# Optimization experiments

Measured on AMD Instinct MI355X. Metric: run time of the kernel, lower is better.

The kernel has to match this reference:

```python
import jax, jax.numpy as jnp
import numpy as np

S, H, W = 64, 294, 518
FOCAL = 300.0


def setup_inputs() -> dict:
    key = jax.random.key(0)
    k1, k2, k3, k4, k5, k6 = jax.random.split(key, 6)
    images = jax.random.uniform(k1, (S, 3, H, W), jnp.float32)
    # sample 3D points inside each camera frustum so most project in-frame
    z = jax.random.uniform(k2, (S, H, W), jnp.float32, 1.0, 5.0)
    x = jax.random.uniform(k3, (S, H, W), jnp.float32, -0.9, 0.9) * z * (W / (2.0 * FOCAL))
    y = jax.random.uniform(k4, (S, H, W), jnp.float32, -0.9, 0.9) * z * (H / (2.0 * FOCAL))
    world_points = jnp.stack([x, y, z], axis=-1)
    world_points_conf = jax.random.uniform(k5, (S, H, W), jnp.float32)
    E = jnp.concatenate([jnp.eye(3, dtype=jnp.float32), jnp.zeros((3, 1), jnp.float32)], axis=1)
    extrinsic = jnp.tile(E[None], (S, 1, 1)) + 0.01 * jax.random.normal(k6, (S, 3, 4), jnp.float32)
    K = jnp.array([[FOCAL, 0.0, W / 2.0], [0.0, FOCAL, H / 2.0], [0.0, 0.0, 1.0]], jnp.float32)
    intrinsic = jnp.tile(K[None], (S, 1, 1))
    return dict(images=images, world_points=world_points,
                world_points_conf=world_points_conf,
                extrinsic=extrinsic, intrinsic=intrinsic)


def reference(images, world_points, world_points_conf, extrinsic, intrinsic):
    s, c, h, w = images.shape
    n = s * h * w
    dtype = images.dtype
    # world -> camera -> pixel (per-frame matmul == torch's gather+bmm since
    # every point's b_idx is its own frame)
    pts_h = jnp.concatenate([world_points, jnp.ones((s, h, w, 1), dtype)], axis=-1)
    cam = jnp.einsum('sij,shwj->shwi', extrinsic, pts_h)          # (S,H,W,3)
    z = cam[..., 2].reshape(n)
    uvh = jnp.einsum('sij,shwj->shwi', intrinsic, cam).reshape(n, 3)
    uv = uvh[:, :2] / (uvh[:, 2:] + 1e-7)
    u, v = uv[:, 0], uv[:, 1]
    valid = (z > 0) & (u >= 0) & (u < w) & (v >= 0) & (v < h)
    u = jnp.clip(u, 0, w - 1)
    v = jnp.clip(v, 0, h - 1)
    u0 = u.astype(jnp.int32)
    v0 = v.astype(jnp.int32)
    u1 = jnp.minimum(u0 + 1, w - 1)
    v1 = jnp.minimum(v0 + 1, h - 1)
    du = u - u0.astype(dtype)
    dv = v - v0.astype(dtype)
    vm = valid.astype(dtype)
    w00 = (1 - du) * (1 - dv) * vm
    w01 = (1 - du) * dv * vm
    w10 = du * (1 - dv) * vm
    w11 = du * dv * vm
    base = jnp.repeat(jnp.arange(s, dtype=jnp.int32), h * w) * (h * w)
    pix_idx = base + v0 * w + u0
    # atomic z-buffer: scatter-min of depth, then hit test
    depth_buf = jnp.full((n,), jnp.inf, jnp.float32).at[pix_idx].min(z)
    hit = ((z == depth_buf[pix_idx]) & valid).astype(dtype)
    rgb = images.transpose(0, 2, 3, 1).reshape(n, 3)
    conf = world_points_conf.reshape(n)
    rgb_buf = jnp.zeros((n, 3), dtype)
    conf_buf = jnp.zeros((n,), dtype)
    for wgt, pu, pv in ((w00, u0, v0), (w01, u0, v1), (w10, u1, v0), (w11, u1, v1)):
        pix = base + pv * w + pu
        wh = wgt * hit
        rgb_buf = rgb_buf.at[pix].add(wh[:, None] * rgb)
        conf_buf = conf_buf.at[pix].add(wh * conf)
    over_exposed = (rgb_buf > 1.0).any(axis=1)
    rgb_buf = jnp.clip(rgb_buf, 0.0, 1.0)
    rgb_map = rgb_buf.reshape(s, h, w, 3).transpose(0, 3, 1, 2)
    depth_map = depth_buf.reshape(s, h, w, 1).transpose(0, 3, 1, 2)
    conf_map = conf_buf.reshape(s, h, w, 1).transpose(0, 3, 1, 2)
    mask_map = ((depth_buf < jnp.inf) & ~over_exposed).reshape(s, 1, h, w).astype(jnp.float32)
    return rgb_map, depth_map, conf_map, mask_map
```

## Files before the change

kernel.cpp:

```cpp
#include <hip/hip_runtime.h>
#include <stdint.h>

constexpr int S = 64, H = 294, W = 518;
constexpr int HW = H * W;
constexpr int N = S * HW;

constexpr int BLK = 256;
constexpr int BPF = (HW + BLK - 1) / BLK;
constexpr int NB  = BPF * S;
constexpr int NXCD = 8;

#define DEPTH_MISS 1.0e30f

typedef unsigned long long u64;
constexpr u64 KEY_SENT = 0xFFFFFFFFFFFFFFFFull;

__device__ __forceinline__ int swz_block() {
  const int orig = blockIdx.x;
  return (orig % NXCD) * (NB / NXCD) + orig / NXCD;
}

__device__ __forceinline__ uint32_t enc_f32(float f) {
  uint32_t u = __float_as_uint(f);
  return (u & 0x80000000u) ? ~u : (u | 0x80000000u);
}
__device__ __forceinline__ float dec_f32(uint32_t u) {
  uint32_t b = (u & 0x80000000u) ? (u ^ 0x80000000u) : ~u;
  return __uint_as_float(b);
}

struct Proj {
  float z, du, dv;
  int u0, v0, u1, v1;
  bool valid;
};

__device__ __forceinline__ Proj project(float px, float py, float pz,
                                        const float* __restrict__ E,
                                        const float* __restrict__ K) {
  Proj r;
  float cx = __fmaf_rn(E[0], px, __fmaf_rn(E[1], py, __fmaf_rn(E[2], pz, E[3])));
  float cy = __fmaf_rn(E[4], px, __fmaf_rn(E[5], py, __fmaf_rn(E[6], pz, E[7])));
  float cz = __fmaf_rn(E[8], px, __fmaf_rn(E[9], py, __fmaf_rn(E[10], pz, E[11])));
  float uh = __fmaf_rn(K[0], cx, __fmaf_rn(K[1], cy, __fmul_rn(K[2], cz)));
  float vh = __fmaf_rn(K[3], cx, __fmaf_rn(K[4], cy, __fmul_rn(K[5], cz)));
  float wh = __fmaf_rn(K[6], cx, __fmaf_rn(K[7], cy, __fmul_rn(K[8], cz)));
  float d  = __fadd_rn(wh, 1e-7f);
  float u  = __fdiv_rn(uh, d);
  float v  = __fdiv_rn(vh, d);
  r.z = cz;
  r.valid = (cz > 0.0f) & (u >= 0.0f) & (u < (float)W) & (v >= 0.0f) & (v < (float)H);
  u = fminf(fmaxf(u, 0.0f), (float)(W - 1));
  v = fminf(fmaxf(v, 0.0f), (float)(H - 1));
  int u0 = (int)u;
  int v0 = (int)v;
  r.u0 = u0; r.v0 = v0;
  r.u1 = min(u0 + 1, W - 1);
  r.v1 = min(v0 + 1, H - 1);
  r.du = __fadd_rn(u, -(float)u0);
  r.dv = __fadd_rn(v, -(float)v0);
  return r;
}


__global__ __launch_bounds__(256) void k_prep(
    const float* __restrict__ wp, const float* __restrict__ extr,
    const float* __restrict__ intr, const float* __restrict__ images,
    const float* __restrict__ conf, u64* __restrict__ keys,
    float4* __restrict__ pack4, float2* __restrict__ pack2) {
  const int wg = swz_block();
  const int s  = wg / BPF;
  const int p  = (wg - s * BPF) * BLK + threadIdx.x;
  if (p >= HW) return;
  const float* E = extr + s * 12;
  const float* K = intr + s * 9;
  const int idx = s * HW + p;
  Proj pr = project(wp[idx*3], wp[idx*3+1], wp[idx*3+2], E, K);
  const int pix = s * HW + pr.v0 * W + pr.u0;
  const u64 key = ((u64)enc_f32(pr.z) << 32) | (uint32_t)p;
  atomicMin(&keys[pix], key);

  const size_t ib = (size_t)s * 3 * HW + p;
  const float vf = pr.valid ? 1.f : 0.f;
  float4 c;
  c.x = vf * images[ib];
  c.y = vf * images[ib + HW];
  c.z = vf * images[ib + 2 * HW];
  c.w = vf * conf[idx];
  pack4[idx] = c;
  pack2[idx] = make_float2(vf * pr.du, vf * pr.dv);
}

__global__ __launch_bounds__(256) void k_gather2(
    const u64* __restrict__ keys, const float4* __restrict__ pack4,
    const float2* __restrict__ pack2, float* __restrict__ out) {
  const int wg = swz_block();
  const int s  = wg / BPF;
  const int p  = (wg - s * BPF) * BLK + threadIdx.x;
  if (p >= HW) return;
  const int y = p / W;
  const int x = p - y * W;
  const bool ex = (x == W - 1);
  const bool ey = (y == H - 1);
  const u64* kfr = keys + (size_t)s * HW;

  const u64 kC = kfr[p];
  const u64 kL = kfr[x > 0 ? p - 1 : p];
  const u64 kU = kfr[y > 0 ? p - W : p];
  const u64 kD = kfr[(x > 0 && y > 0) ? p - W - 1 : p];

  const float fC = (kC != KEY_SENT) ? 1.f : 0.f;
  const float fL = (x > 0 && kL != KEY_SENT) ? 1.f : 0.f;
  const float fU = (y > 0 && kU != KEY_SENT) ? 1.f : 0.f;
  const float fD = (x > 0 && y > 0 && kD != KEY_SENT) ? 1.f : 0.f;

  const int base = s * HW;
  const int pC = base + (kC == KEY_SENT ? 0 : (int)(uint32_t)kC);
  const int pL = base + (kL == KEY_SENT ? 0 : (int)(uint32_t)kL);
  const int pU = base + (kU == KEY_SENT ? 0 : (int)(uint32_t)kU);
  const int pD = base + (kD == KEY_SENT ? 0 : (int)(uint32_t)kD);

  const float4 cC = pack4[pC], cL = pack4[pL], cU = pack4[pU], cD = pack4[pD];
  const float2 dC = pack2[pC], dL = pack2[pL], dU = pack2[pU], dD = pack2[pD];

  const float wC = fC * (ex ? 1.f : 1.f - dC.x) * (ey ? 1.f : 1.f - dC.y);
  const float wL = fL * dL.x * (ey ? 1.f : 1.f - dL.y);
  const float wU = fU * (ex ? 1.f : 1.f - dU.x) * dU.y;
  const float wD = fD * dD.x * dD.y;

  const float ar = wC * cC.x + wU * cU.x + wL * cL.x + wD * cD.x;
  const float ag = wC * cC.y + wU * cU.y + wL * cL.y + wD * cD.y;
  const float ab = wC * cC.z + wU * cU.z + wL * cL.z + wD * cD.z;
  const float ac = wC * cC.w + wU * cU.w + wL * cL.w + wD * cD.w;

  const bool over = (ar > 1.f) | (ag > 1.f) | (ab > 1.f);

  float* rgb   = out;
  float* depth = out + (size_t)3 * N;
  float* cbuf  = out + (size_t)4 * N;
  float* mask  = out + (size_t)5 * N;

  const size_t ob = (size_t)s * 3 * HW + p;
  rgb[ob]          = fminf(fmaxf(ar, 0.f), 1.f);
  rgb[ob + HW]     = fminf(fmaxf(ag, 0.f), 1.f);
  rgb[ob + 2 * HW] = fminf(fmaxf(ab, 0.f), 1.f);

  const int i = s * HW + p;
  const bool missed = (kC == KEY_SENT);
  depth[i] = missed ? DEPTH_MISS : dec_f32((uint32_t)(kC >> 32));
  cbuf[i]  = ac;
  mask[i]  = (!missed && !over) ? 1.f : 0.f;
}


__global__ __launch_bounds__(256) void k_depth64(
    const float* __restrict__ wp, const float* __restrict__ extr,
    const float* __restrict__ intr, u64* __restrict__ keys) {
  const int wg = swz_block();
  const int s  = wg / BPF;
  const int p  = (wg - s * BPF) * BLK + threadIdx.x;
  if (p >= HW) return;
  const float* E = extr + s * 12;
  const float* K = intr + s * 9;
  const int idx = s * HW + p;
  Proj pr = project(wp[idx*3], wp[idx*3+1], wp[idx*3+2], E, K);
  const int pix = s * HW + pr.v0 * W + pr.u0;
  const u64 key = ((u64)enc_f32(pr.z) << 32) | (uint32_t)p;
  atomicMin(&keys[pix], key);
}

__global__ __launch_bounds__(256) void k_gather(
    const float* __restrict__ wp, const float* __restrict__ extr,
    const float* __restrict__ intr, const float* __restrict__ images,
    const float* __restrict__ conf, const u64* __restrict__ keys,
    float* __restrict__ out) {
  const int wg = swz_block();
  const int s  = wg / BPF;
  const int p  = (wg - s * BPF) * BLK + threadIdx.x;
  if (p >= HW) return;
  const int y = p / W;
  const int x = p - y * W;
  const float* E = extr + s * 12;
  const float* K = intr + s * 9;
  const u64* kfr = keys + (size_t)s * HW;
  const float* img = images + (size_t)s * 3 * HW;
  const float* cfp = conf + (size_t)s * HW;
  const bool ex = (x == W - 1);
  const bool ey = (y == H - 1);

  float ar = 0.f, ag = 0.f, ab = 0.f, ac = 0.f;
  const u64 k0 = kfr[p];

  auto contrib = [&](u64 k, int role) {
    if (k == KEY_SENT) return;
    const int pid = (int)(uint32_t)k;
    const float* q = wp + ((size_t)s * HW + pid) * 3;
    Proj pr = project(q[0], q[1], q[2], E, K);
    if (!pr.valid) return;
    const float du = pr.du, dv = pr.dv;
    float wgt;
    if (role == 0)      wgt = (ex ? 1.f : 1.f - du) * (ey ? 1.f : 1.f - dv);
    else if (role == 1) wgt = du * (ey ? 1.f : 1.f - dv);
    else if (role == 2) wgt = (ex ? 1.f : 1.f - du) * dv;
    else                wgt = du * dv;
    if (wgt == 0.f) return;
    ar += wgt * img[pid];
    ag += wgt * img[HW + pid];
    ab += wgt * img[2 * HW + pid];
    ac += wgt * cfp[pid];
  };

  contrib(k0, 0);
  if (x > 0)          contrib(kfr[p - 1], 1);
  if (y > 0)          contrib(kfr[p - W], 2);
  if (x > 0 && y > 0) contrib(kfr[p - W - 1], 3);

  const bool over = (ar > 1.f) | (ag > 1.f) | (ab > 1.f);

  float* rgb   = out;
  float* depth = out + (size_t)3 * N;
  float* cbuf  = out + (size_t)4 * N;
  float* mask  = out + (size_t)5 * N;

  const size_t ob = (size_t)s * 3 * HW + p;
  rgb[ob]          = fminf(fmaxf(ar, 0.f), 1.f);
  rgb[ob + HW]     = fminf(fmaxf(ag, 0.f), 1.f);
  rgb[ob + 2 * HW] = fminf(fmaxf(ab, 0.f), 1.f);

  const int i = s * HW + p;
  const bool missed = (k0 == KEY_SENT);
  depth[i] = missed ? DEPTH_MISS : dec_f32((uint32_t)(k0 >> 32));
  cbuf[i]  = ac;
  mask[i]  = (!missed && !over) ? 1.f : 0.f;
}


__global__ __launch_bounds__(256) void k_depth(
    const float* __restrict__ wp, const float* __restrict__ extr,
    const float* __restrict__ intr, uint32_t* __restrict__ denc) {
  const int s = blockIdx.y;
  const int p = blockIdx.x * blockDim.x + threadIdx.x;
  if (p >= HW) return;
  const float* E = extr + s * 12;
  const float* K = intr + s * 9;
  const int idx = s * HW + p;
  Proj pr = project(wp[idx*3], wp[idx*3+1], wp[idx*3+2], E, K);
  const int pix = s * HW + pr.v0 * W + pr.u0;
  atomicMin(&denc[pix], enc_f32(pr.z));
}

__global__ __launch_bounds__(256) void k_splat(
    const float* __restrict__ wp, const float* __restrict__ extr,
    const float* __restrict__ intr, const float* __restrict__ images,
    const float* __restrict__ conf, const uint32_t* __restrict__ denc,
    float* __restrict__ rgb_buf, float* __restrict__ conf_buf) {
  const int s = blockIdx.y;
  const int p = blockIdx.x * blockDim.x + threadIdx.x;
  if (p >= HW) return;
  const float* E = extr + s * 12;
  const float* K = intr + s * 9;
  const int idx = s * HW + p;
  Proj pr = project(wp[idx*3], wp[idx*3+1], wp[idx*3+2], E, K);
  const int pix0 = s * HW + pr.v0 * W + pr.u0;
  if (!pr.valid) return;
  if (enc_f32(pr.z) != denc[pix0]) return;

  const float du = pr.du, dv = pr.dv;
  const float w00 = (1.0f - du) * (1.0f - dv);
  const float w01 = (1.0f - du) * dv;
  const float w10 = du * (1.0f - dv);
  const float w11 = du * dv;

  const int ibase = s * 3 * HW + p;
  const float r = images[ibase];
  const float g = images[ibase + HW];
  const float b = images[ibase + 2 * HW];
  const float cf = conf[idx];
  const int sbase = s * HW;
  const int cbase = s * 3 * HW;

  #define SPLAT(WGT, PU, PV)                                              \
    if ((WGT) != 0.0f) {                                                  \
      const int q = (PV) * W + (PU);                                      \
      unsafeAtomicAdd(&rgb_buf[cbase + q],          (WGT) * r);           \
      unsafeAtomicAdd(&rgb_buf[cbase + HW + q],     (WGT) * g);           \
      unsafeAtomicAdd(&rgb_buf[cbase + 2 * HW + q], (WGT) * b);           \
      unsafeAtomicAdd(&conf_buf[sbase + q],         (WGT) * cf);          \
    }
  SPLAT(w00, pr.u0, pr.v0)
  SPLAT(w01, pr.u0, pr.v1)
  SPLAT(w10, pr.u1, pr.v0)
  SPLAT(w11, pr.u1, pr.v1)
  #undef SPLAT
}

__global__ __launch_bounds__(256) void k_final(float* __restrict__ out) {
  const int s = blockIdx.y;
  const int p = blockIdx.x * blockDim.x + threadIdx.x;
  if (p >= HW) return;
  float* rgb = out;
  float* depth = out + (size_t)3 * N;
  float* mask = out + (size_t)5 * N;
  uint32_t* denc = (uint32_t*)depth;

  const int cbase = s * 3 * HW + p;
  const float r = rgb[cbase];
  const float g = rgb[cbase + HW];
  const float b = rgb[cbase + 2 * HW];
  const bool over = (r > 1.0f) | (g > 1.0f) | (b > 1.0f);
  rgb[cbase]          = fminf(fmaxf(r, 0.0f), 1.0f);
  rgb[cbase + HW]     = fminf(fmaxf(g, 0.0f), 1.0f);
  rgb[cbase + 2 * HW] = fminf(fmaxf(b, 0.0f), 1.0f);

  const int i = s * HW + p;
  const uint32_t u = denc[i];
  const bool missed = (u == 0xFFFFFFFFu);
  depth[i] = missed ? DEPTH_MISS : dec_f32(u);
  mask[i] = (!missed && !over) ? 1.0f : 0.0f;
}

extern "C" void kernel_launch(void* const* d_in, const int* in_sizes, int n_in,
                              void* d_out, int out_size, void* d_ws, size_t ws_size,
                              hipStream_t stream) {
  const float* images = (const float*)d_in[0];
  const float* wp     = (const float*)d_in[1];
  const float* conf   = (const float*)d_in[2];
  const float* extr   = (const float*)d_in[3];
  const float* intr   = (const float*)d_in[4];
  float* out = (float*)d_out;

  const size_t keys_bytes  = (size_t)N * sizeof(u64);
  const size_t pack4_bytes = (size_t)N * sizeof(float4);
  const size_t pack2_bytes = (size_t)N * sizeof(float2);
  dim3 blk(BLK, 1, 1);

  if (ws_size >= keys_bytes + pack4_bytes + pack2_bytes) {
    u64*    keys  = (u64*)d_ws;
    float4* pack4 = (float4*)((char*)d_ws + keys_bytes);
    float2* pack2 = (float2*)((char*)d_ws + keys_bytes + pack4_bytes);
    hipMemsetAsync(keys, 0xFF, keys_bytes, stream);
    dim3 grd(NB, 1, 1);
    hipLaunchKernelGGL(k_prep, grd, blk, 0, stream, wp, extr, intr, images,
                       conf, keys, pack4, pack2);
    hipLaunchKernelGGL(k_gather2, grd, blk, 0, stream, keys, pack4, pack2, out);
  } else if (ws_size >= keys_bytes) {
    u64* keys = (u64*)d_ws;
    hipMemsetAsync(keys, 0xFF, keys_bytes, stream);
    dim3 grd(NB, 1, 1);
    hipLaunchKernelGGL(k_depth64, grd, blk, 0, stream, wp, extr, intr, keys);
    hipLaunchKernelGGL(k_gather, grd, blk, 0, stream, wp, extr, intr, images,
                       conf, keys, out);
  } else {
    float*    rgb_buf  = out;
    uint32_t* denc     = (uint32_t*)(out + (size_t)3 * N);
    float*    conf_buf = out + (size_t)4 * N;
    hipMemsetAsync(rgb_buf, 0, (size_t)3 * N * sizeof(float), stream);
    hipMemsetAsync(denc, 0xFF, (size_t)N * sizeof(uint32_t), stream);
    hipMemsetAsync(conf_buf, 0, (size_t)N * sizeof(float), stream);
    dim3 grd(BPF, S, 1);
    hipLaunchKernelGGL(k_depth, grd, blk, 0, stream, wp, extr, intr, denc);
    hipLaunchKernelGGL(k_splat, grd, blk, 0, stream, wp, extr, intr, images,
                       conf, denc, rgb_buf, conf_buf);
    hipLaunchKernelGGL(k_final, grd, blk, 0, stream, out);
  }
}
```

Baseline: 687.1 us.

## Share neighbor gathers via LDS and interleave per-point records into 24-byte AoS

The gather kernel now has each thread fetch the z-buffer winner record for its own pixel and the pixel one row up, and stores both in shared memory. Left and diagonal neighbours are then read from LDS, so each block does about two random gathers per pixel instead of four. The separate float4 and float2 pack arrays are merged into one interleaved 24-byte record per point, so one gather touches a single contiguous region. The cost is a __syncthreads, a halo fill by the last thread, and 8-byte-aligned loads in place of 16-byte ones.

```diff
diff --git a/kernel.cpp b/kernel.cpp
--- a/kernel.cpp
+++ b/kernel.cpp
@@ -67,7 +67,7 @@
     const float* __restrict__ wp, const float* __restrict__ extr,
     const float* __restrict__ intr, const float* __restrict__ images,
     const float* __restrict__ conf, u64* __restrict__ keys,
-    float4* __restrict__ pack4, float2* __restrict__ pack2) {
+    float2* __restrict__ rec) {
   const int wg = swz_block();
   const int s  = wg / BPF;
   const int p  = (wg - s * BPF) * BLK + threadIdx.x;
@@ -82,51 +82,80 @@
 
   const size_t ib = (size_t)s * 3 * HW + p;
   const float vf = pr.valid ? 1.f : 0.f;
-  float4 c;
-  c.x = vf * images[ib];
-  c.y = vf * images[ib + HW];
-  c.z = vf * images[ib + 2 * HW];
-  c.w = vf * conf[idx];
-  pack4[idx] = c;
-  pack2[idx] = make_float2(vf * pr.du, vf * pr.dv);
-}
-
-__global__ __launch_bounds__(256) void k_gather2(
-    const u64* __restrict__ keys, const float4* __restrict__ pack4,
-    const float2* __restrict__ pack2, float* __restrict__ out) {
+  float2* r2 = rec + (size_t)idx * 3;
+  r2[0] = make_float2(vf * images[ib],          vf * images[ib + HW]);
+  r2[1] = make_float2(vf * images[ib + 2 * HW], vf * conf[idx]);
+  r2[2] = make_float2(vf * pr.du,               vf * pr.dv);
+}
+
+__global__ __launch_bounds__(256) void k_gather3(
+    const u64* __restrict__ keys, const float2* __restrict__ rec,
+    float* __restrict__ out) {
+  __shared__ float4   eC[BLK + 1];
+  __shared__ float2   dC[BLK + 1];
+  __shared__ float4   eU[BLK + 1];
+  __shared__ float2   dU[BLK + 1];
+  __shared__ uint32_t hC[BLK + 1];
+
   const int wg = swz_block();
   const int s  = wg / BPF;
-  const int p  = (wg - s * BPF) * BLK + threadIdx.x;
+  const int p0 = (wg - s * BPF) * BLK;
+  const int t  = threadIdx.x;
+  const u64* kfr = keys + (size_t)s * HW;
+  const float2* rfr = rec + (size_t)s * HW * 3;
+
+  auto fill = [&](int slot, int q) {
+    float4 c  = make_float4(0.f, 0.f, 0.f, 0.f);
+    float2 d  = make_float2(0.f, 0.f);
+    float4 cu = make_float4(0.f, 0.f, 0.f, 0.f);
+    float2 du2 = make_float2(0.f, 0.f);
+    uint32_t hi = 0xFFFFFFFFu;
+    if (q >= 0 && q < HW) {
+      const u64 k = kfr[q];
+      if (k != KEY_SENT) {
+        hi = (uint32_t)(k >> 32);
+        const float2* r2 = rfr + (size_t)(uint32_t)k * 3;
+        const float2 a = r2[0], b = r2[1], e = r2[2];
+        c = make_float4(a.x, a.y, b.x, b.y);
+        d = e;
+      }
+      const int qU = q - W;
+      if (qU >= 0) {
+        const u64 ku = kfr[qU];
+        if (ku != KEY_SENT) {
+          const float2* r2 = rfr + (size_t)(uint32_t)ku * 3;
+          const float2 a = r2[0], b = r2[1], e = r2[2];
+          cu = make_float4(a.x, a.y, b.x, b.y);
+          du2 = e;
+        }
+      }
+    }
+    eC[slot] = c;  dC[slot] = d;  hC[slot] = hi;
+    eU[slot] = cu; dU[slot] = du2;
+  };
+
+  fill(t, p0 - 1 + t);
+  if (t == BLK - 1) fill(BLK, p0 + BLK - 1);
+  __syncthreads();
+
+  const int p = p0 + t;
   if (p >= HW) return;
   const int y = p / W;
   const int x = p - y * W;
   const bool ex = (x == W - 1);
   const bool ey = (y == H - 1);
-  const u64* kfr = keys + (size_t)s * HW;
-
-  const u64 kC = kfr[p];
-  const u64 kL = kfr[x > 0 ? p - 1 : p];
-  const u64 kU = kfr[y > 0 ? p - W : p];
-  const u64 kD = kfr[(x > 0 && y > 0) ? p - W - 1 : p];
-
-  const float fC = (kC != KEY_SENT) ? 1.f : 0.f;
-  const float fL = (x > 0 && kL != KEY_SENT) ? 1.f : 0.f;
-  const float fU = (y > 0 && kU != KEY_SENT) ? 1.f : 0.f;
-  const float fD = (x > 0 && y > 0 && kD != KEY_SENT) ? 1.f : 0.f;
-
-  const int base = s * HW;
-  const int pC = base + (kC == KEY_SENT ? 0 : (int)(uint32_t)kC);
-  const int pL = base + (kL == KEY_SENT ? 0 : (int)(uint32_t)kL);
-  const int pU = base + (kU == KEY_SENT ? 0 : (int)(uint32_t)kU);
-  const int pD = base + (kD == KEY_SENT ? 0 : (int)(uint32_t)kD);
-
-  const float4 cC = pack4[pC], cL = pack4[pL], cU = pack4[pU], cD = pack4[pD];
-  const float2 dC = pack2[pC], dL = pack2[pL], dU = pack2[pU], dD = pack2[pD];
-
-  const float wC = fC * (ex ? 1.f : 1.f - dC.x) * (ey ? 1.f : 1.f - dC.y);
-  const float wL = fL * dL.x * (ey ? 1.f : 1.f - dL.y);
-  const float wU = fU * (ex ? 1.f : 1.f - dU.x) * dU.y;
-  const float wD = fD * dD.x * dD.y;
+  const float gx = (x > 0) ? 1.f : 0.f;
+
+  const float4 cC = eC[t + 1]; const float2 ddC = dC[t + 1];
+  const float4 cU = eU[t + 1]; const float2 ddU = dU[t + 1];
+  const float4 cL = eC[t];     const float2 ddL = dC[t];
+  const float4 cD = eU[t];     const float2 ddD = dU[t];
+  const uint32_t hi = hC[t + 1];
+
+  const float wC = (ex ? 1.f : 1.f - ddC.x) * (ey ? 1.f : 1.f - ddC.y);
+  const float wU = (ex ? 1.f : 1.f - ddU.x) * ddU.y;
+  const float wL = gx * ddL.x * (ey ? 1.f : 1.f - ddL.y);
+  const float wD = gx * ddD.x * ddD.y;
 
   const float ar = wC * cC.x + wU * cU.x + wL * cL.x + wD * cD.x;
   const float ag = wC * cC.y + wU * cU.y + wL * cL.y + wD * cD.y;
@@ -146,8 +175,8 @@
   rgb[ob + 2 * HW] = fminf(fmaxf(ab, 0.f), 1.f);
 
   const int i = s * HW + p;
-  const bool missed = (kC == KEY_SENT);
-  depth[i] = missed ? DEPTH_MISS : dec_f32((uint32_t)(kC >> 32));
+  const bool missed = (hi == 0xFFFFFFFFu);
+  depth[i] = missed ? DEPTH_MISS : dec_f32(hi);
   cbuf[i]  = ac;
   mask[i]  = (!missed && !over) ? 1.f : 0.f;
 }
@@ -329,20 +358,18 @@
   const float* intr   = (const float*)d_in[4];
   float* out = (float*)d_out;
 
-  const size_t keys_bytes  = (size_t)N * sizeof(u64);
-  const size_t pack4_bytes = (size_t)N * sizeof(float4);
-  const size_t pack2_bytes = (size_t)N * sizeof(float2);
+  const size_t keys_bytes = (size_t)N * sizeof(u64);
+  const size_t rec_bytes  = (size_t)N * 6 * sizeof(float);
   dim3 blk(BLK, 1, 1);
 
-  if (ws_size >= keys_bytes + pack4_bytes + pack2_bytes) {
-    u64*    keys  = (u64*)d_ws;
-    float4* pack4 = (float4*)((char*)d_ws + keys_bytes);
-    float2* pack2 = (float2*)((char*)d_ws + keys_bytes + pack4_bytes);
+  if (ws_size >= keys_bytes + rec_bytes) {
+    u64*    keys = (u64*)d_ws;
+    float2* rec  = (float2*)((char*)d_ws + keys_bytes);
     hipMemsetAsync(keys, 0xFF, keys_bytes, stream);
     dim3 grd(NB, 1, 1);
     hipLaunchKernelGGL(k_prep, grd, blk, 0, stream, wp, extr, intr, images,
-                       conf, keys, pack4, pack2);
-    hipLaunchKernelGGL(k_gather2, grd, blk, 0, stream, keys, pack4, pack2, out);
+                       conf, keys, rec);
+    hipLaunchKernelGGL(k_gather3, grd, blk, 0, stream, keys, rec, out);
   } else if (ws_size >= keys_bytes) {
     u64* keys = (u64*)d_ws;
     hipMemsetAsync(keys, 0xFF, keys_bytes, stream);
```

New measurement: 585.4 us. -14.8%, faster.
